# Performance work log

Hardware: AMD Instinct MI355X
Metric: run time of the kernel (lower is better)

## Reference

```python
import jax, jax.numpy as jnp
import numpy as np

B, L, D = 32, 256, 512
D_STATE, D_CONV, EXPAND, NODE_DIM, D_FF = 16, 4, 2, 16, 2048
D_INNER = EXPAND * D
DT_RANK = D // 16


def _layernorm(x, g, b, eps=1e-5):
    mu = x.mean(-1, keepdims=True)
    var = ((x - mu) ** 2).mean(-1, keepdims=True)
    return (x - mu) * jax.lax.rsqrt(var + eps) * g + b


def _mamba(x, in_w, conv_w, conv_b, xproj_w, dt_w, dt_b, A_log, Dp, out_w):
    # Standard selective-scan (S6) Mamba inner block.
    Bb, Ll, _ = x.shape
    u, z = jnp.split(x @ in_w, 2, axis=-1)                # (B,L,d_inner) each
    pad = jnp.pad(u, ((0, 0), (D_CONV - 1, 0), (0, 0)))   # causal depthwise conv1d
    u = sum(pad[:, k:k + Ll, :] * conv_w[:, k] for k in range(D_CONV)) + conv_b
    u = jax.nn.silu(u)
    proj = u @ xproj_w                                    # (B,L,dt_rank+2*d_state)
    dt, Bm, Cm = jnp.split(proj, [DT_RANK, DT_RANK + D_STATE], axis=-1)
    dt = jax.nn.softplus(dt @ dt_w + dt_b)                # (B,L,d_inner)
    A = -jnp.exp(A_log)                                   # (d_inner,d_state)
    dA = jnp.exp(dt[..., None] * A)                       # (B,L,d_inner,d_state)
    dBu = dt[..., None] * Bm[:, :, None, :] * u[..., None]

    def step(h, inp):
        dA_t, dBu_t, C_t = inp
        h = dA_t * h + dBu_t
        return h, jnp.einsum('bds,bs->bd', h, C_t)

    h0 = jnp.zeros((Bb, D_INNER, D_STATE), x.dtype)
    _, ys = jax.lax.scan(step, h0, (dA.transpose(1, 0, 2, 3),
                                    dBu.transpose(1, 0, 2, 3),
                                    Cm.transpose(1, 0, 2)))
    y = ys.transpose(1, 0, 2) + u * Dp                    # (B,L,d_inner)
    return (y * jax.nn.silu(z)) @ out_w


def _forward(x,
             d_in_w, d_conv_w, d_conv_b, d_xproj_w, d_dt_w, d_dt_b, d_A_log, d_D, d_out_w, d_ln_g, d_ln_b,
             s_emb1, s_emb2, s_in_w, s_conv_w, s_conv_b, s_xproj_w, s_dt_w, s_dt_b, s_A_log, s_D, s_out_w, s_ln_g, s_ln_b,
             f_ln_g, f_ln_b, f_w1, f_b1, f_w2, f_b2):
    # DiffSSM: selective SSM on the first-differenced sequence, residual + LN
    xd = jnp.concatenate([x[:, :1], x[:, 1:] - x[:, :-1]], axis=1)
    x = _layernorm(x + _mamba(xd, d_in_w, d_conv_w, d_conv_b, d_xproj_w,
                              d_dt_w, d_dt_b, d_A_log, d_D, d_out_w),
                   d_ln_g, d_ln_b)
    # SpatialGraphMamba: learned adjacency over enc_in tokens, graph mix, SSM
    adj = jax.nn.softmax(jax.nn.relu(s_emb1 @ s_emb2.T), axis=-1)  # (enc_in,enc_in)
    xg = jnp.einsum('nl,bld->bnd', adj, x)
    x = _layernorm(x + _mamba(xg, s_in_w, s_conv_w, s_conv_b, s_xproj_w,
                              s_dt_w, s_dt_b, s_A_log, s_D, s_out_w),
                   s_ln_g, s_ln_b)
    # Pre-norm FFN with residual
    h = _layernorm(x, f_ln_g, f_ln_b)
    x = x + jax.nn.gelu(h @ f_w1 + f_b1) @ f_w2 + f_b2
    return x, adj


def setup_inputs() -> dict:
    key = jax.random.key(0)
    ks = iter(jax.random.split(key, 64))

    def rn(shape, s=0.02):
        return jax.random.normal(next(ks), shape, jnp.float32) * s

    A_log_init = jnp.log(jnp.broadcast_to(
        jnp.arange(1, D_STATE + 1, dtype=jnp.float32), (D_INNER, D_STATE)))
    dt_b_init = jnp.full((D_INNER,), -4.6, jnp.float32)  # softplus^-1(~0.01)

    inp = {'x': jax.random.normal(next(ks), (B, L, D), jnp.float32)}
    for p in ('d_', 's_'):
        inp[p + 'in_w'] = rn((D, 2 * D_INNER))
        inp[p + 'conv_w'] = rn((D_INNER, D_CONV), 0.1)
        inp[p + 'conv_b'] = jnp.zeros((D_INNER,), jnp.float32)
        inp[p + 'xproj_w'] = rn((D_INNER, DT_RANK + 2 * D_STATE))
        inp[p + 'dt_w'] = rn((DT_RANK, D_INNER))
        inp[p + 'dt_b'] = dt_b_init
        inp[p + 'A_log'] = A_log_init
        inp[p + 'D'] = jnp.ones((D_INNER,), jnp.float32)
        inp[p + 'out_w'] = rn((D_INNER, D))
        inp[p + 'ln_g'] = jnp.ones((D,), jnp.float32)
        inp[p + 'ln_b'] = jnp.zeros((D,), jnp.float32)
    inp['s_emb1'] = rn((L, NODE_DIM), 0.1)
    inp['s_emb2'] = rn((L, NODE_DIM), 0.1)
    inp['f_ln_g'] = jnp.ones((D,), jnp.float32)
    inp['f_ln_b'] = jnp.zeros((D,), jnp.float32)
    inp['f_w1'] = rn((D, D_FF))
    inp['f_b1'] = jnp.zeros((D_FF,), jnp.float32)
    inp['f_w2'] = rn((D_FF, D))
    inp['f_b2'] = jnp.zeros((D,), jnp.float32)
    return inp


def reference(x,
              d_in_w, d_conv_w, d_conv_b, d_xproj_w, d_dt_w, d_dt_b, d_A_log, d_D, d_out_w, d_ln_g, d_ln_b,
              s_emb1, s_emb2, s_in_w, s_conv_w, s_conv_b, s_xproj_w, s_dt_w, s_dt_b, s_A_log, s_D, s_out_w, s_ln_g, s_ln_b,
              f_ln_g, f_ln_b, f_w1, f_b1, f_w2, f_b2):
    return _forward(x,
                    d_in_w, d_conv_w, d_conv_b, d_xproj_w, d_dt_w, d_dt_b, d_A_log, d_D, d_out_w, d_ln_g, d_ln_b,
                    s_emb1, s_emb2, s_in_w, s_conv_w, s_conv_b, s_xproj_w, s_dt_w, s_dt_b, s_A_log, s_D, s_out_w, s_ln_g, s_ln_b,
                    f_ln_g, f_ln_b, f_w1, f_b1, f_w2, f_b2)
```

## Files before the change

### kernel.cpp

```cpp
#include <hip/hip_runtime.h>

#define DEV __device__ __forceinline__

typedef __bf16 bf16x8 __attribute__((ext_vector_type(8)));
typedef float  f32x4  __attribute__((ext_vector_type(4)));

DEV unsigned short f2b(float f) {
    union { float f; unsigned u; } v; v.f = f;
    unsigned r = v.u + 0x7fffu + ((v.u >> 16) & 1u);
    return (unsigned short)(r >> 16);
}
DEV float b2f(unsigned short h) {
    union { unsigned u; float f; } v; v.u = ((unsigned)h) << 16;
    return v.f;
}
DEV float sigmoidf_(float x) { return 1.f / (1.f + __expf(-x)); }
DEV float geluf_(float x) {
    float t = 0.7978845608028654f * (x + 0.044715f * x * x * x);
    return 0.5f * x * (1.f + tanhf(t));
}
DEV float softplusf_(float x) { return x > 15.f ? x : log1pf(__expf(x)); }
DEV void gload_lds16(const void* g, void* l) {
    __builtin_amdgcn_global_load_lds((const __attribute__((address_space(1))) void*)g,
                                     (__attribute__((address_space(3))) void*)l, 16, 0, 0);
}


struct WtDesc { const float* s; unsigned short* d; int K; int N; int t0; };
struct WtArgs { WtDesc m[12]; };

__global__ __launch_bounds__(256) void wtrans_k(WtArgs a) {
    __shared__ float tile[32][33];
    int t = blockIdx.x;
    int mi = 0;
#pragma unroll
    for (int j = 1; j < 12; j++) if (t >= a.m[j].t0) mi = j;
    const float* src0 = a.m[mi].s;
    unsigned short* dst0 = a.m[mi].d;
    const int K = a.m[mi].K, N = a.m[mi].N;
    const int lt = t - a.m[mi].t0;
    const int ntk = K >> 5;
    const int kt = lt % ntk, nt = lt / ntk;
    const int c = threadIdx.x & 31, r = threadIdx.x >> 5;
    const float* src = src0 + (size_t)(kt * 32) * N + nt * 32;
#pragma unroll
    for (int i = 0; i < 4; i++) tile[r + i * 8][c] = src[(size_t)(r + i * 8) * N + c];
    __syncthreads();
    unsigned short* dst = dst0 + (size_t)(nt * 32) * K + kt * 32;
#pragma unroll
    for (int i = 0; i < 4; i++) dst[(size_t)(r + i * 8) * K + c] = f2b(tile[c][r + i * 8]);
}

__global__ __launch_bounds__(256) void diff_k(const float* __restrict__ x,
                                              unsigned short* __restrict__ xd) {
    size_t i4 = (size_t)blockIdx.x * 256 + threadIdx.x;
    size_t idx = i4 * 4;
    int l = (int)((idx >> 9) & 255);
    float4 v = *(const float4*)&x[idx];
    if (l > 0) {
        float4 p = *(const float4*)&x[idx - 512];
        v.x -= p.x; v.y -= p.y; v.z -= p.z; v.w -= p.w;
    }
    unsigned short o[4] = {f2b(v.x), f2b(v.y), f2b(v.z), f2b(v.w)};
    *(unsigned long long*)&xd[idx] = *(unsigned long long*)o;
}

__global__ __launch_bounds__(256) void adj_k(const float* __restrict__ e1,
                                             const float* __restrict__ e2,
                                             float* __restrict__ adjf,
                                             unsigned short* __restrict__ adjb) {
    const int n = blockIdx.x, tid = threadIdx.x;
    __shared__ float e1s[16];
    __shared__ float redm[4], reds[4];
    if (tid < 16) e1s[tid] = e1[n * 16 + tid];
    __syncthreads();
    const float* e2r = e2 + tid * 16;
    float dot = 0.f;
#pragma unroll
    for (int k = 0; k < 16; k++) dot = fmaf(e1s[k], e2r[k], dot);
    float v = fmaxf(dot, 0.f);
    float m = v;
#pragma unroll
    for (int o = 32; o > 0; o >>= 1) m = fmaxf(m, __shfl_xor(m, o));
    const int lane = tid & 63, wv = tid >> 6;
    if (lane == 0) redm[wv] = m;
    __syncthreads();
    m = fmaxf(fmaxf(redm[0], redm[1]), fmaxf(redm[2], redm[3]));
    float e = __expf(v - m);
    float ssum = e;
#pragma unroll
    for (int o = 32; o > 0; o >>= 1) ssum += __shfl_xor(ssum, o);
    if (lane == 0) reds[wv] = ssum;
    __syncthreads();
    ssum = reds[0] + reds[1] + reds[2] + reds[3];
    float o = e / ssum;
    adjf[(size_t)n * 256 + tid] = o;
    adjb[(size_t)n * 256 + tid] = f2b(o);
}

template<int HBIAS, int HGELU>
__global__ __launch_bounds__(512, 2) void gemm256_k(
    const unsigned short* __restrict__ A, const unsigned short* __restrict__ Bt,
    unsigned short* __restrict__ C, const float* __restrict__ bias,
    int M, int N, int K, int lda) {
    constexpr int BM = 256, BN = 256, BK = 64;
    __shared__ __align__(16) unsigned short As[2][BM * BK];
    __shared__ __align__(16) unsigned short Bs[2][BN * BK];
    const int tid  = threadIdx.x;
    const int lane = tid & 63;
    const int wave = tid >> 6;
    const int wr = wave >> 2;
    const int wc = wave & 3;
    const int bm = blockIdx.x * BM, bn = blockIdx.y * BN;
    const int lrow  = lane & 15;
    const int klane = lane >> 4;

    f32x4 acc[8][4];
#pragma unroll
    for (int m = 0; m < 8; m++)
#pragma unroll
        for (int n = 0; n < 4; n++) {
            acc[m][n][0] = 0.f; acc[m][n][1] = 0.f; acc[m][n][2] = 0.f; acc[m][n][3] = 0.f;
        }

    auto STAGE = [&](int buf, int k0) {
#pragma unroll
        for (int it = 0; it < 4; ++it) {
            int flat = (it * 512 + tid) * 8;
            int r = flat >> 6, s = (flat & 63) >> 3;
            int c = (s ^ (r & 7)) * 8;
            gload_lds16(A + (size_t)(bm + r) * lda + (k0 + c),
                        &As[buf][(it * 512 + (tid & 448)) * 8]);
        }
#pragma unroll
        for (int it = 0; it < 4; ++it) {
            int flat = (it * 512 + tid) * 8;
            int r = flat >> 6, s = (flat & 63) >> 3;
            int c = (s ^ (r & 7)) * 8;
            gload_lds16(Bt + (size_t)(bn + r) * K + (k0 + c),
                        &Bs[buf][(it * 512 + (tid & 448)) * 8]);
        }
    };
    auto COMPUTE = [&](int buf) {
#pragma unroll
        for (int kk = 0; kk < 2; kk++) {
            bf16x8 af[8], bfv[4];
#pragma unroll
            for (int m = 0; m < 8; m++) {
                int rr = wr * 128 + m * 16 + lrow;
                int sl = (kk * 4 + klane) ^ (rr & 7);
                af[m] = *(const bf16x8*)&As[buf][rr * BK + sl * 8];
            }
#pragma unroll
            for (int n = 0; n < 4; n++) {
                int rr = wc * 64 + n * 16 + lrow;
                int sl = (kk * 4 + klane) ^ (rr & 7);
                bfv[n] = *(const bf16x8*)&Bs[buf][rr * BK + sl * 8];
            }
#pragma unroll
            for (int m = 0; m < 8; m++)
#pragma unroll
                for (int n = 0; n < 4; n++)
                    acc[m][n] = __builtin_amdgcn_mfma_f32_16x16x32_bf16(af[m], bfv[n], acc[m][n], 0, 0, 0);
        }
    };

    const int nt = K / BK;
    STAGE(0, 0);
    __syncthreads();
    for (int t = 0; t < nt; t += 2) {
        if (t + 1 < nt) STAGE(1, (t + 1) * BK);
        COMPUTE(0);
        __syncthreads();
        if (t + 1 < nt) {
            if (t + 2 < nt) STAGE(0, (t + 2) * BK);
            COMPUTE(1);
            if (t + 2 < nt) __syncthreads();
        }
    }

    const int r0 = (lane >> 4) << 2;
    unsigned short* Cs = As[0];
    constexpr int PITCH = BN + 8;
#pragma unroll
    for (int g = 0; g < 8; g++) {
        __syncthreads();
        if (wr == (g >> 2)) {
#pragma unroll
            for (int mm = 0; mm < 2; mm++) {
                const int m = (g & 3) * 2 + mm;
#pragma unroll
                for (int n = 0; n < 4; n++) {
                    const int cl = wc * 64 + n * 16 + lrow;
                    float bv = HBIAS ? bias[bn + cl] : 0.f;
#pragma unroll
                    for (int j = 0; j < 4; j++) {
                        float v = acc[m][n][j] + bv;
                        if (HGELU) v = geluf_(v);
                        Cs[(mm * 16 + r0 + j) * PITCH + cl] = f2b(v);
                    }
                }
            }
        }
        __syncthreads();
#pragma unroll
        for (int i = 0; i < 2; i++) {
            int flat = (i * 512 + tid) * 8;
            int row = flat >> 8, col = flat & 255;
            uint4 val = *(const uint4*)&Cs[row * PITCH + col];
            *(uint4*)&C[(size_t)(bm + g * 32 + row) * N + bn + col] = val;
        }
    }
}

template<int BM, int BN, int BK, int WRN, int FM, int FN,
         int OBF, int HBIAS, int HGELU, int HRES, int HSP>
__global__ __launch_bounds__(256) void gemm_k(
    const unsigned short* __restrict__ A, const unsigned short* __restrict__ Bt,
    void* __restrict__ C, const float* __restrict__ bias, const float* __restrict__ res,
    int M, int N, int K, int lda, long sA, long sB, long sC) {
    constexpr int SMASK = BK / 8 - 1;
    constexpr int KH    = BK / 32;
    __shared__ __align__(16) unsigned short As[BM * BK];
    __shared__ __align__(16) unsigned short Bs[BN * BK];
    const int tid  = threadIdx.x;
    const int lane = tid & 63;
    const int wave = tid >> 6;
    const int wr = wave / WRN, wc = wave % WRN;
    const int bm = blockIdx.x * BM, bn = blockIdx.y * BN;
    const unsigned short* Ab = A  + (size_t)blockIdx.z * sA;
    const unsigned short* Bb = Bt + (size_t)blockIdx.z * sB;
    const int lrow  = lane & 15;
    const int klane = lane >> 4;

    f32x4 acc[FM][FN];
#pragma unroll
    for (int m = 0; m < FM; m++)
#pragma unroll
        for (int n = 0; n < FN; n++) {
            acc[m][n][0] = 0.f; acc[m][n][1] = 0.f; acc[m][n][2] = 0.f; acc[m][n][3] = 0.f;
        }

    constexpr int AI = (BM * BK) / 2048;
    constexpr int BI = (BN * BK) / 2048;

    for (int k0 = 0; k0 < K; k0 += BK) {
#pragma unroll
        for (int it = 0; it < AI; ++it) {
            int flat = (it * 256 + tid) * 8;
            int r = flat / BK, s = (flat % BK) >> 3;
            int c = (s ^ (r & SMASK)) * 8;
            gload_lds16(Ab + (size_t)(bm + r) * lda + (k0 + c),
                        &As[(it * 256 + (tid & 192)) * 8]);
        }
#pragma unroll
        for (int it = 0; it < BI; ++it) {
            int flat = (it * 256 + tid) * 8;
            int r = flat / BK, s = (flat % BK) >> 3;
            int c = (s ^ (r & SMASK)) * 8;
            gload_lds16(Bb + (size_t)(bn + r) * K + (k0 + c),
                        &Bs[(it * 256 + (tid & 192)) * 8]);
        }
        __syncthreads();
#pragma unroll
        for (int kk = 0; kk < KH; kk++) {
            bf16x8 af[FM], bfv[FN];
#pragma unroll
            for (int m = 0; m < FM; m++) {
                int rr = wr * FM * 16 + m * 16 + lrow;
                int sl = (kk * 4 + klane) ^ (rr & SMASK);
                af[m] = *(const bf16x8*)&As[rr * BK + sl * 8];
            }
#pragma unroll
            for (int n = 0; n < FN; n++) {
                int rr = wc * FN * 16 + n * 16 + lrow;
                int sl = (kk * 4 + klane) ^ (rr & SMASK);
                bfv[n] = *(const bf16x8*)&Bs[rr * BK + sl * 8];
            }
#pragma unroll
            for (int m = 0; m < FM; m++)
#pragma unroll
                for (int n = 0; n < FN; n++)
                    acc[m][n] = __builtin_amdgcn_mfma_f32_16x16x32_bf16(af[m], bfv[n], acc[m][n], 0, 0, 0);
        }
        __syncthreads();
    }

    const int r0 = (lane >> 4) << 2;
    if (OBF) {
        unsigned short* Cs = Bs;
        constexpr int PITCH = BN + 8;
        unsigned short* Cg = (unsigned short*)C;
#pragma unroll
        for (int g = 0; g < BM / 32; g++) {
            __syncthreads();
            if (wr == (g * 2) / FM) {
                const int mb = (g * 2) % FM;
#pragma unroll
                for (int mm = 0; mm < 2; mm++) {
#pragma unroll
                    for (int n = 0; n < FN; n++) {
                        const int cl = wc * FN * 16 + n * 16 + lrow;
                        float bv = HBIAS ? bias[bn + cl] : 0.f;
#pragma unroll
                        for (int j = 0; j < 4; j++) {
                            float v = acc[mb + mm][n][j] + bv;
                            if (HSP)   v = softplusf_(v);
                            if (HGELU) v = geluf_(v);
                            Cs[(mm * 16 + r0 + j) * PITCH + cl] = f2b(v);
                        }
                    }
                }
            }
            __syncthreads();
#pragma unroll
            for (int i = 0; i < (32 * BN) / 2048; i++) {
                int flat = (i * 256 + tid) * 8;
                int row = flat / BN, col = flat % BN;
                uint4 val = *(const uint4*)&Cs[row * PITCH + col];
                size_t oi = (size_t)blockIdx.z * sC + (size_t)(bm + g * 32 + row) * N + bn + col;
                *(uint4*)&Cg[oi] = val;
            }
        }
    } else {
#pragma unroll
        for (int n = 0; n < FN; n++) {
            const int ccol = bn + wc * FN * 16 + n * 16 + lrow;
            float bv = HBIAS ? bias[ccol] : 0.f;
#pragma unroll
            for (int m = 0; m < FM; m++) {
#pragma unroll
                for (int j = 0; j < 4; j++) {
                    const int rrow = bm + wr * FM * 16 + m * 16 + r0 + j;
                    float v = acc[m][n][j] + bv;
                    if (HSP)   v = softplusf_(v);
                    if (HGELU) v = geluf_(v);
                    if (HRES)  v += res[(size_t)rrow * N + ccol];
                    ((float*)C)[(size_t)blockIdx.z * sC + (size_t)rrow * N + ccol] = v;
                }
            }
        }
    }
}

__global__ __launch_bounds__(256) void conv_k(const unsigned short* __restrict__ uz,
                                              const float* __restrict__ w,
                                              const float* __restrict__ cb,
                                              unsigned short* __restrict__ u) {
    int t = blockIdx.x * 256 + threadIdx.x;
    int dg = t & 127;
    int r4 = t >> 7;
    int l0 = (r4 & 63) * 4;
    size_t row0 = (size_t)r4 * 4;
    int d0 = dg * 8;

    float4 wv[8];
#pragma unroll
    for (int j = 0; j < 8; j++) wv[j] = ((const float4*)w)[d0 + j];
    float cbv[8];
#pragma unroll
    for (int j = 0; j < 8; j++) cbv[j] = cb[d0 + j];

    uint4 rows[7];
#pragma unroll
    for (int i = 0; i < 7; i++) {
        int ls = l0 + i - 3;
        if (ls >= 0) rows[i] = *(const uint4*)(uz + ((row0 + i - 3) << 11) + d0);
        else         rows[i] = make_uint4(0u, 0u, 0u, 0u);
    }

#pragma unroll
    for (int o = 0; o < 4; o++) {
        float acc[8];
#pragma unroll
        for (int j = 0; j < 8; j++) acc[j] = cbv[j];
#pragma unroll
        for (int k = 0; k < 4; k++) {
            const unsigned short* vs = (const unsigned short*)&rows[o + k];
            const float* wk = (const float*)&wv[0];
#pragma unroll
            for (int j = 0; j < 8; j++)
                acc[j] = fmaf(((const float*)&wv[j])[k], b2f(vs[j]), acc[j]);
            (void)wk;
        }
        unsigned short ob[8];
#pragma unroll
        for (int j = 0; j < 8; j++) {
            float a = acc[j];
            ob[j] = f2b(a * sigmoidf_(a));
        }
        *(uint4*)(u + ((row0 + o) << 10) + d0) = *(const uint4*)ob;
    }
}

__global__ __launch_bounds__(256) void scan1_k(
    const float* __restrict__ dt,
    const unsigned short* __restrict__ u,
    const unsigned short* __restrict__ proj,
    const float* __restrict__ A_log,
    float* __restrict__ hend, float* __restrict__ Sc) {
    const int dg = blockIdx.x, c = blockIdx.y, b = blockIdx.z;
    const int d = dg * 256 + threadIdx.x;
    const size_t base = (size_t)b * 256 + c * 32;
    __shared__ float Bs[32][16];
    for (int i = threadIdx.x; i < 512; i += 256) {
        int r = i >> 4, s = i & 15;
        Bs[r][s] = b2f(proj[(base + r) * 64 + 32 + s]);
    }
    __syncthreads();
    float Aa[16];
#pragma unroll
    for (int s = 0; s < 16; s++) Aa[s] = -__expf(A_log[d * 16 + s]);
    float h[16];
#pragma unroll
    for (int s = 0; s < 16; s++) h[s] = 0.f;
    float ssum = 0.f;
    for (int l = 0; l < 32; l++) {
        size_t row = base + l;
        float dtv = dt[(row << 10) + d];
        float uu  = b2f(u[(row << 10) + d]);
        float du  = dtv * uu;
        ssum += dtv;
#pragma unroll
        for (int s = 0; s < 16; s++)
            h[s] = __expf(dtv * Aa[s]) * h[s] + du * Bs[l][s];
    }
    size_t o = (size_t)(b * 8 + c) * 1024 + d;
    Sc[o] = ssum;
#pragma unroll
    for (int s = 0; s < 16; s++) hend[o * 16 + s] = h[s];
}

__global__ __launch_bounds__(256) void scan2_k(
    const float* __restrict__ hend, const float* __restrict__ Sc,
    const float* __restrict__ A_log, float* __restrict__ hstart) {
    const int d = blockIdx.x * 256 + threadIdx.x;
    const int b = blockIdx.y;
    float Aa[16];
#pragma unroll
    for (int s = 0; s < 16; s++) Aa[s] = -__expf(A_log[d * 16 + s]);
    float h[16];
#pragma unroll
    for (int s = 0; s < 16; s++) h[s] = 0.f;
    for (int c = 0; c < 8; c++) {
        size_t o = (size_t)(b * 8 + c) * 1024 + d;
#pragma unroll
        for (int s = 0; s < 16; s++) hstart[o * 16 + s] = h[s];
        float sc = Sc[o];
#pragma unroll
        for (int s = 0; s < 16; s++)
            h[s] = __expf(sc * Aa[s]) * h[s] + hend[o * 16 + s];
    }
}

__global__ __launch_bounds__(256) void scan3_k(
    const float* __restrict__ dt,
    const unsigned short* __restrict__ u,
    const unsigned short* __restrict__ uz,
    const unsigned short* __restrict__ proj,
    const float* __restrict__ A_log,
    const float* __restrict__ Dp,
    const float* __restrict__ hstart,
    unsigned short* __restrict__ yg) {
    const int dg = blockIdx.x, c = blockIdx.y, b = blockIdx.z;
    const int d = dg * 256 + threadIdx.x;
    const size_t base = (size_t)b * 256 + c * 32;
    __shared__ float BCs[32][32];
    for (int i = threadIdx.x; i < 1024; i += 256) {
        int r = i >> 5, s = i & 31;
        BCs[r][s] = b2f(proj[(base + r) * 64 + 32 + s]);
    }
    __syncthreads();
    float Aa[16];
#pragma unroll
    for (int s = 0; s < 16; s++) Aa[s] = -__expf(A_log[d * 16 + s]);
    const float Dd = Dp[d];
    float h[16];
    size_t ho = ((size_t)(b * 8 + c) * 1024 + d) * 16;
#pragma unroll
    for (int s = 0; s < 16; s++) h[s] = hstart[ho + s];
    for (int l = 0; l < 32; l++) {
        size_t row = base + l;
        float dtv = dt[(row << 10) + d];
        float uu  = b2f(u[(row << 10) + d]);
        float zz  = b2f(uz[(row << 11) + 1024 + d]);
        float du  = dtv * uu;
        float y = 0.f;
#pragma unroll
        for (int s = 0; s < 16; s++) {
            h[s] = __expf(dtv * Aa[s]) * h[s] + du * BCs[l][s];
            y = fmaf(h[s], BCs[l][16 + s], y);
        }
        y = fmaf(uu, Dd, y);
        yg[(row << 10) + d] = f2b(y * (zz * sigmoidf_(zz)));
    }
}

template<int HRES, int OF32, int OBF>
__global__ __launch_bounds__(256) void ln_k(const float* __restrict__ xin,
                                            const float* __restrict__ resin,
                                            const float* __restrict__ g,
                                            const float* __restrict__ b,
                                            float* __restrict__ outf,
                                            unsigned short* __restrict__ outb) {
    const int row = blockIdx.x, tid = threadIdx.x;
    float2 v = ((const float2*)(xin + (size_t)row * 512))[tid];
    if (HRES) {
        float2 r2 = ((const float2*)(resin + (size_t)row * 512))[tid];
        v.x += r2.x; v.y += r2.y;
    }
    float s = v.x + v.y, q = v.x * v.x + v.y * v.y;
#pragma unroll
    for (int o = 32; o > 0; o >>= 1) { s += __shfl_xor(s, o); q += __shfl_xor(q, o); }
    __shared__ float sm[4], qm[4];
    const int lane = tid & 63, wv = tid >> 6;
    if (lane == 0) { sm[wv] = s; qm[wv] = q; }
    __syncthreads();
    s = sm[0] + sm[1] + sm[2] + sm[3];
    q = qm[0] + qm[1] + qm[2] + qm[3];
    const float mu = s * (1.f / 512.f);
    const float ri = rsqrtf(q * (1.f / 512.f) - mu * mu + 1e-5f);
    float2 gg = ((const float2*)g)[tid];
    float2 bb = ((const float2*)b)[tid];
    float o0 = (v.x - mu) * ri * gg.x + bb.x;
    float o1 = (v.y - mu) * ri * gg.y + bb.y;
    if (OF32) ((float2*)(outf + (size_t)row * 512))[tid] = make_float2(o0, o1);
    if (OBF) {
        unsigned short* ob = outb + (size_t)row * 512 + tid * 2;
        ob[0] = f2b(o0); ob[1] = f2b(o1);
    }
}

__global__ __launch_bounds__(256) void trans_k(const float* __restrict__ x1,
                                               unsigned short* __restrict__ xt) {
    __shared__ float tile[32][33];
    const int b = blockIdx.z;
    const int d0 = blockIdx.x * 32, l0 = blockIdx.y * 32;
    const int c = threadIdx.x & 31, r = threadIdx.x >> 5;
    const float* src = x1 + ((size_t)b * 256 + l0) * 512 + d0;
#pragma unroll
    for (int i = 0; i < 4; i++) tile[r + i * 8][c] = src[(size_t)(r + i * 8) * 512 + c];
    __syncthreads();
    unsigned short* dst = xt + ((size_t)b * 512 + d0) * 256 + l0;
#pragma unroll
    for (int i = 0; i < 4; i++) dst[(size_t)(r + i * 8) * 256 + c] = f2b(tile[c][r + i * 8]);
}

constexpr size_t OFF_WT_DIN  = 0;
constexpr size_t OFF_WT_SIN  = OFF_WT_DIN  + 2048ull * 512 * 2;
constexpr size_t OFF_WT_DOUT = OFF_WT_SIN  + 2048ull * 512 * 2;
constexpr size_t OFF_WT_SOUT = OFF_WT_DOUT + 512ull * 1024 * 2;
constexpr size_t OFF_WT_F1   = OFF_WT_SOUT + 512ull * 1024 * 2;
constexpr size_t OFF_WT_F2   = OFF_WT_F1   + 2048ull * 512 * 2;
constexpr size_t OFF_XPT_D   = OFF_WT_F2   + 512ull * 2048 * 2;
constexpr size_t OFF_XPT_S   = OFF_XPT_D   + 64ull * 1024 * 2;
constexpr size_t OFF_DTT_D   = OFF_XPT_S   + 64ull * 1024 * 2;
constexpr size_t OFF_DTT_S   = OFF_DTT_D   + 1024ull * 32 * 2;
constexpr size_t OFF_ACT     = OFF_DTT_S   + 1024ull * 32 * 2;
constexpr size_t OFF_UZ      = OFF_ACT  + 8192ull * 512 * 2;
constexpr size_t OFF_U       = OFF_UZ   + 8192ull * 2048 * 2;
constexpr size_t OFF_PROJ    = OFF_U    + 8192ull * 1024 * 2;
constexpr size_t OFF_YG      = OFF_PROJ + 8192ull * 64 * 2;
constexpr size_t OFF_MOUT    = OFF_YG   + 8192ull * 1024 * 2;
constexpr size_t OFF_X1      = OFF_MOUT + 8192ull * 512 * 4;
constexpr size_t OFF_X2      = OFF_X1   + 8192ull * 512 * 4;
constexpr size_t OFF_X1T     = OFF_X2   + 8192ull * 512 * 4;
constexpr size_t OFF_ADJB    = OFF_X1T  + 32ull * 512 * 256 * 2;
constexpr size_t OFF_DT      = OFF_ADJB + 256ull * 256 * 2;
constexpr size_t OFF_HST     = OFF_DT   + 8192ull * 1024 * 4;
constexpr size_t OFF_SC      = OFF_HST  + 32ull * 8 * 1024 * 16 * 4;

extern "C" void kernel_launch(void* const* d_in, const int* in_sizes, int n_in,
                              void* d_out, int out_size, void* d_ws, size_t ws_size,
                              hipStream_t stream) {
    (void)in_sizes; (void)n_in; (void)out_size; (void)ws_size;
    const float* x      = (const float*)d_in[0];
    const float* dinw   = (const float*)d_in[1];
    const float* dconvw = (const float*)d_in[2];
    const float* dconvb = (const float*)d_in[3];
    const float* dxproj = (const float*)d_in[4];
    const float* ddtw   = (const float*)d_in[5];
    const float* ddtb   = (const float*)d_in[6];
    const float* dAlog  = (const float*)d_in[7];
    const float* dD     = (const float*)d_in[8];
    const float* doutw  = (const float*)d_in[9];
    const float* dlng   = (const float*)d_in[10];
    const float* dlnb   = (const float*)d_in[11];
    const float* sinw   = (const float*)d_in[12];
    const float* sconvw = (const float*)d_in[13];
    const float* sconvb = (const float*)d_in[14];
    const float* sxproj = (const float*)d_in[15];
    const float* sdtw   = (const float*)d_in[16];
    const float* sdtb   = (const float*)d_in[17];
    const float* sAlog  = (const float*)d_in[18];
    const float* sD     = (const float*)d_in[19];
    const float* soutw  = (const float*)d_in[20];
    const float* slng   = (const float*)d_in[21];
    const float* slnb   = (const float*)d_in[22];
    const float* semb1  = (const float*)d_in[23];
    const float* semb2  = (const float*)d_in[24];
    const float* flng   = (const float*)d_in[25];
    const float* flnb   = (const float*)d_in[26];
    const float* fw1    = (const float*)d_in[27];
    const float* fb1    = (const float*)d_in[28];
    const float* fw2    = (const float*)d_in[29];
    const float* fb2    = (const float*)d_in[30];

    char* ws = (char*)d_ws;
    unsigned short* wtDin  = (unsigned short*)(ws + OFF_WT_DIN);
    unsigned short* wtSin  = (unsigned short*)(ws + OFF_WT_SIN);
    unsigned short* wtDout = (unsigned short*)(ws + OFF_WT_DOUT);
    unsigned short* wtSout = (unsigned short*)(ws + OFF_WT_SOUT);
    unsigned short* wtF1   = (unsigned short*)(ws + OFF_WT_F1);
    unsigned short* wtF2   = (unsigned short*)(ws + OFF_WT_F2);
    unsigned short* xptD   = (unsigned short*)(ws + OFF_XPT_D);
    unsigned short* xptS   = (unsigned short*)(ws + OFF_XPT_S);
    unsigned short* dttD   = (unsigned short*)(ws + OFF_DTT_D);
    unsigned short* dttS   = (unsigned short*)(ws + OFF_DTT_S);
    unsigned short* actIn  = (unsigned short*)(ws + OFF_ACT);
    unsigned short* uzBuf  = (unsigned short*)(ws + OFF_UZ);
    unsigned short* uBuf   = (unsigned short*)(ws + OFF_U);
    unsigned short* projB  = (unsigned short*)(ws + OFF_PROJ);
    unsigned short* ygBuf  = (unsigned short*)(ws + OFF_YG);
    float*          moutB  = (float*)(ws + OFF_MOUT);
    float*          hendB  = moutB;
    float*          x1Buf  = (float*)(ws + OFF_X1);
    float*          x2Buf  = (float*)(ws + OFF_X2);
    unsigned short* x1tBuf = (unsigned short*)(ws + OFF_X1T);
    unsigned short* adjB   = (unsigned short*)(ws + OFF_ADJB);
    float*          dtBuf  = (float*)(ws + OFF_DT);
    float*          hstB   = (float*)(ws + OFF_HST);
    float*          scB    = (float*)(ws + OFF_SC);
    unsigned short* hBuf   = uBuf;
    unsigned short* midBuf = uzBuf;

    float* outX   = (float*)d_out;
    float* outAdj = outX + 4194304;

    WtArgs wa;
    wa.m[0]  = WtDesc{dinw,   wtDin,  512,  2048, 0};
    wa.m[1]  = WtDesc{sinw,   wtSin,  512,  2048, 1024};
    wa.m[2]  = WtDesc{doutw,  wtDout, 1024, 512,  2048};
    wa.m[3]  = WtDesc{soutw,  wtSout, 1024, 512,  2560};
    wa.m[4]  = WtDesc{fw1,    wtF1,   512,  2048, 3072};
    wa.m[5]  = WtDesc{fw2,    wtF2,   2048, 512,  4096};
    wa.m[6]  = WtDesc{dxproj, xptD,   1024, 64,   5120};
    wa.m[7]  = WtDesc{sxproj, xptS,   1024, 64,   5184};
    wa.m[8]  = WtDesc{ddtw,   dttD,   32,   1024, 5248};
    wa.m[9]  = WtDesc{sdtw,   dttS,   32,   1024, 5280};
    wa.m[10] = WtDesc{dinw,   wtDin,  512,  2048, 0x7fffffff};
    wa.m[11] = WtDesc{dinw,   wtDin,  512,  2048, 0x7fffffff};
    wtrans_k<<<dim3(5312), dim3(256), 0, stream>>>(wa);

    diff_k<<<dim3(4096), dim3(256), 0, stream>>>(x, actIn);
    adj_k<<<dim3(256), dim3(256), 0, stream>>>(semb1, semb2, outAdj, adjB);

    gemm256_k<0,0><<<dim3(32,8), dim3(512), 0, stream>>>(
        actIn, wtDin, uzBuf, nullptr, 8192, 2048, 512, 512);
    conv_k<<<dim3(1024), dim3(256), 0, stream>>>(uzBuf, dconvw, dconvb, uBuf);
    gemm_k<64,64,64,2,2,2, 1,0,0,0,0><<<dim3(128,1,1), dim3(256), 0, stream>>>(
        uBuf, xptD, projB, nullptr, nullptr, 8192, 64, 1024, 1024, 0, 0, 0);
    gemm_k<128,128,32,2,4,4, 0,1,0,0,1><<<dim3(64,8,1), dim3(256), 0, stream>>>(
        projB, dttD, dtBuf, ddtb, nullptr, 8192, 1024, 32, 64, 0, 0, 0);
    scan1_k<<<dim3(4,8,32), dim3(256), 0, stream>>>(dtBuf, uBuf, projB, dAlog, hendB, scB);
    scan2_k<<<dim3(4,32),   dim3(256), 0, stream>>>(hendB, scB, dAlog, hstB);
    scan3_k<<<dim3(4,8,32), dim3(256), 0, stream>>>(dtBuf, uBuf, uzBuf, projB, dAlog, dD, hstB, ygBuf);
    gemm_k<128,128,64,2,4,4, 0,0,0,1,0><<<dim3(64,4,1), dim3(256), 0, stream>>>(
        ygBuf, wtDout, moutB, nullptr, x, 8192, 512, 1024, 1024, 0, 0, 0);
    ln_k<0,1,0><<<dim3(8192), dim3(256), 0, stream>>>(moutB, nullptr, dlng, dlnb, x1Buf, nullptr);

    trans_k<<<dim3(16,8,32), dim3(256), 0, stream>>>(x1Buf, x1tBuf);
    gemm_k<128,128,64,2,4,4, 1,0,0,0,0><<<dim3(2,4,32), dim3(256), 0, stream>>>(
        adjB, x1tBuf, actIn, nullptr, nullptr, 256, 512, 256, 256, 0, 131072, 131072);
    gemm256_k<0,0><<<dim3(32,8), dim3(512), 0, stream>>>(
        actIn, wtSin, uzBuf, nullptr, 8192, 2048, 512, 512);
    conv_k<<<dim3(1024), dim3(256), 0, stream>>>(uzBuf, sconvw, sconvb, uBuf);
    gemm_k<64,64,64,2,2,2, 1,0,0,0,0><<<dim3(128,1,1), dim3(256), 0, stream>>>(
        uBuf, xptS, projB, nullptr, nullptr, 8192, 64, 1024, 1024, 0, 0, 0);
    gemm_k<128,128,32,2,4,4, 0,1,0,0,1><<<dim3(64,8,1), dim3(256), 0, stream>>>(
        projB, dttS, dtBuf, sdtb, nullptr, 8192, 1024, 32, 64, 0, 0, 0);
    scan1_k<<<dim3(4,8,32), dim3(256), 0, stream>>>(dtBuf, uBuf, projB, sAlog, hendB, scB);
    scan2_k<<<dim3(4,32),   dim3(256), 0, stream>>>(hendB, scB, sAlog, hstB);
    scan3_k<<<dim3(4,8,32), dim3(256), 0, stream>>>(dtBuf, uBuf, uzBuf, projB, sAlog, sD, hstB, ygBuf);
    gemm_k<128,128,64,2,4,4, 0,0,0,1,0><<<dim3(64,4,1), dim3(256), 0, stream>>>(
        ygBuf, wtSout, moutB, nullptr, x1Buf, 8192, 512, 1024, 1024, 0, 0, 0);
    ln_k<0,1,0><<<dim3(8192), dim3(256), 0, stream>>>(moutB, nullptr, slng, slnb, x2Buf, nullptr);

    ln_k<0,0,1><<<dim3(8192), dim3(256), 0, stream>>>(x2Buf, nullptr, flng, flnb, nullptr, hBuf);
    gemm256_k<1,1><<<dim3(32,8), dim3(512), 0, stream>>>(
        hBuf, wtF1, midBuf, fb1, 8192, 2048, 512, 512);
    gemm_k<128,128,64,2,4,4, 0,1,0,1,0><<<dim3(64,4,1), dim3(256), 0, stream>>>(
        midBuf, wtF2, outX, fb2, x2Buf, 8192, 512, 2048, 2048, 0, 0, 0);
}
```

Measured before the change: 540.7 us.

## Split-K the x_proj GEMM across eight slices with a separate reduce kernel

The narrow x_proj GEMM (N=64, K=1024) previously launched only 128 blocks. It now splits K into eight slices to launch 1024 blocks, writing fp32 partials into the dt scratch buffer. A new reduction kernel sums the partials and converts the result to bf16. To support this, the GEMM kernel gains an explicit B leading-dimension argument. The trade is extra partial-sum memory traffic and one more launch per Mamba block in exchange for better occupancy.

New measurement: 538.1 us. No clear change (-0.5%).

```diff
diff --git a/kernel.cpp b/kernel.cpp
--- a/kernel.cpp
+++ b/kernel.cpp
@@ -218,7 +218,7 @@
 __global__ __launch_bounds__(256) void gemm_k(
     const unsigned short* __restrict__ A, const unsigned short* __restrict__ Bt,
     void* __restrict__ C, const float* __restrict__ bias, const float* __restrict__ res,
-    int M, int N, int K, int lda, long sA, long sB, long sC) {
+    int M, int N, int K, int lda, int ldb, long sA, long sB, long sC) {
     constexpr int SMASK = BK / 8 - 1;
     constexpr int KH    = BK / 32;
     __shared__ __align__(16) unsigned short As[BM * BK];
@@ -258,7 +258,7 @@
             int flat = (it * 256 + tid) * 8;
             int r = flat / BK, s = (flat % BK) >> 3;
             int c = (s ^ (r & SMASK)) * 8;
-            gload_lds16(Bb + (size_t)(bn + r) * K + (k0 + c),
+            gload_lds16(Bb + (size_t)(bn + r) * ldb + (k0 + c),
                         &Bs[(it * 256 + (tid & 192)) * 8]);
         }
         __syncthreads();
@@ -343,6 +343,20 @@
     }
 }
 
+__global__ __launch_bounds__(256) void xred_k(const float* __restrict__ p,
+                                              unsigned short* __restrict__ o) {
+    int i = blockIdx.x * 256 + threadIdx.x;
+    const float4* p4 = (const float4*)p;
+    float4 s = p4[i];
+#pragma unroll
+    for (int z = 1; z < 8; z++) {
+        float4 t = p4[z * 131072 + i];
+        s.x += t.x; s.y += t.y; s.z += t.z; s.w += t.w;
+    }
+    unsigned short ob[4] = {f2b(s.x), f2b(s.y), f2b(s.z), f2b(s.w)};
+    *(unsigned long long*)&o[(size_t)i * 4] = *(unsigned long long*)ob;
+}
+
 __global__ __launch_bounds__(256) void conv_k(const unsigned short* __restrict__ uz,
                                               const float* __restrict__ w,
                                               const float* __restrict__ cb,
@@ -377,11 +391,9 @@
 #pragma unroll
         for (int k = 0; k < 4; k++) {
             const unsigned short* vs = (const unsigned short*)&rows[o + k];
-            const float* wk = (const float*)&wv[0];
 #pragma unroll
             for (int j = 0; j < 8; j++)
                 acc[j] = fmaf(((const float*)&wv[j])[k], b2f(vs[j]), acc[j]);
-            (void)wk;
         }
         unsigned short ob[8];
 #pragma unroll
@@ -629,6 +641,7 @@
     unsigned short* x1tBuf = (unsigned short*)(ws + OFF_X1T);
     unsigned short* adjB   = (unsigned short*)(ws + OFF_ADJB);
     float*          dtBuf  = (float*)(ws + OFF_DT);
+    float*          xppBuf = dtBuf;
     float*          hstB   = (float*)(ws + OFF_HST);
     float*          scB    = (float*)(ws + OFF_SC);
     unsigned short* hBuf   = uBuf;
@@ -658,37 +671,39 @@
     gemm256_k<0,0><<<dim3(32,8), dim3(512), 0, stream>>>(
         actIn, wtDin, uzBuf, nullptr, 8192, 2048, 512, 512);
     conv_k<<<dim3(1024), dim3(256), 0, stream>>>(uzBuf, dconvw, dconvb, uBuf);
-    gemm_k<64,64,64,2,2,2, 1,0,0,0,0><<<dim3(128,1,1), dim3(256), 0, stream>>>(
-        uBuf, xptD, projB, nullptr, nullptr, 8192, 64, 1024, 1024, 0, 0, 0);
+    gemm_k<64,64,64,2,2,2, 0,0,0,0,0><<<dim3(128,1,8), dim3(256), 0, stream>>>(
+        uBuf, xptD, xppBuf, nullptr, nullptr, 8192, 64, 128, 1024, 1024, 128, 128, 524288);
+    xred_k<<<dim3(512), dim3(256), 0, stream>>>(xppBuf, projB);
     gemm_k<128,128,32,2,4,4, 0,1,0,0,1><<<dim3(64,8,1), dim3(256), 0, stream>>>(
-        projB, dttD, dtBuf, ddtb, nullptr, 8192, 1024, 32, 64, 0, 0, 0);
+        projB, dttD, dtBuf, ddtb, nullptr, 8192, 1024, 32, 64, 32, 0, 0, 0);
     scan1_k<<<dim3(4,8,32), dim3(256), 0, stream>>>(dtBuf, uBuf, projB, dAlog, hendB, scB);
     scan2_k<<<dim3(4,32),   dim3(256), 0, stream>>>(hendB, scB, dAlog, hstB);
     scan3_k<<<dim3(4,8,32), dim3(256), 0, stream>>>(dtBuf, uBuf, uzBuf, projB, dAlog, dD, hstB, ygBuf);
     gemm_k<128,128,64,2,4,4, 0,0,0,1,0><<<dim3(64,4,1), dim3(256), 0, stream>>>(
-        ygBuf, wtDout, moutB, nullptr, x, 8192, 512, 1024, 1024, 0, 0, 0);
+        ygBuf, wtDout, moutB, nullptr, x, 8192, 512, 1024, 1024, 1024, 0, 0, 0);
     ln_k<0,1,0><<<dim3(8192), dim3(256), 0, stream>>>(moutB, nullptr, dlng, dlnb, x1Buf, nullptr);
 
     trans_k<<<dim3(16,8,32), dim3(256), 0, stream>>>(x1Buf, x1tBuf);
     gemm_k<128,128,64,2,4,4, 1,0,0,0,0><<<dim3(2,4,32), dim3(256), 0, stream>>>(
-        adjB, x1tBuf, actIn, nullptr, nullptr, 256, 512, 256, 256, 0, 131072, 131072);
+        adjB, x1tBuf, actIn, nullptr, nullptr, 256, 512, 256, 256, 256, 0, 131072, 131072);
     gemm256_k<0,0><<<dim3(32,8), dim3(512), 0, stream>>>(
         actIn, wtSin, uzBuf, nullptr, 8192, 2048, 512, 512);
     conv_k<<<dim3(1024), dim3(256), 0, stream>>>(uzBuf, sconvw, sconvb, uBuf);
-    gemm_k<64,64,64,2,2,2, 1,0,0,0,0><<<dim3(128,1,1), dim3(256), 0, stream>>>(
-        uBuf, xptS, projB, nullptr, nullptr, 8192, 64, 1024, 1024, 0, 0, 0);
+    gemm_k<64,64,64,2,2,2, 0,0,0,0,0><<<dim3(128,1,8), dim3(256), 0, stream>>>(
+        uBuf, xptS, xppBuf, nullptr, nullptr, 8192, 64, 128, 1024, 1024, 128, 128, 524288);
+    xred_k<<<dim3(512), dim3(256), 0, stream>>>(xppBuf, projB);
     gemm_k<128,128,32,2,4,4, 0,1,0,0,1><<<dim3(64,8,1), dim3(256), 0, stream>>>(
-        projB, dttS, dtBuf, sdtb, nullptr, 8192, 1024, 32, 64, 0, 0, 0);
+        projB, dttS, dtBuf, sdtb, nullptr, 8192, 1024, 32, 64, 32, 0, 0, 0);
     scan1_k<<<dim3(4,8,32), dim3(256), 0, stream>>>(dtBuf, uBuf, projB, sAlog, hendB, scB);
     scan2_k<<<dim3(4,32),   dim3(256), 0, stream>>>(hendB, scB, sAlog, hstB);
     scan3_k<<<dim3(4,8,32), dim3(256), 0, stream>>>(dtBuf, uBuf, uzBuf, projB, sAlog, sD, hstB, ygBuf);
     gemm_k<128,128,64,2,4,4, 0,0,0,1,0><<<dim3(64,4,1), dim3(256), 0, stream>>>(
-        ygBuf, wtSout, moutB, nullptr, x1Buf, 8192, 512, 1024, 1024, 0, 0, 0);
+        ygBuf, wtSout, moutB, nullptr, x1Buf, 8192, 512, 1024, 1024, 1024, 0, 0, 0);
     ln_k<0,1,0><<<dim3(8192), dim3(256), 0, stream>>>(moutB, nullptr, slng, slnb, x2Buf, nullptr);
 
     ln_k<0,0,1><<<dim3(8192), dim3(256), 0, stream>>>(x2Buf, nullptr, flng, flnb, nullptr, hBuf);
     gemm256_k<1,1><<<dim3(32,8), dim3(512), 0, stream>>>(
         hBuf, wtF1, midBuf, fb1, 8192, 2048, 512, 512);
     gemm_k<128,128,64,2,4,4, 0,1,0,1,0><<<dim3(64,4,1), dim3(256), 0, stream>>>(
-        midBuf, wtF2, outX, fb2, x2Buf, 8192, 512, 2048, 2048, 0, 0, 0);
-}
+        midBuf, wtF2, outX, fb2, x2Buf, 8192, 512, 2048, 2048, 2048, 0, 0, 0);
+}
```
